# Kernel optimization log

Measured on AMD Instinct MI355X. Metric: run time of the kernel, lower is better.

## Reference

```python
import jax, jax.numpy as jnp
import numpy as np

B, CIN, CF, FH, FW = 16, 512, 64, 11, 20
N = 2784          # anchors
NOFF = 72         # S offsets
D = CF * FH       # 704

def setup_inputs() -> dict:
    key = jax.random.key(0)
    ks = jax.random.split(key, 12)
    x = jax.random.normal(ks[0], (B, CIN, FH, FW), jnp.float32)
    conv_w = jax.random.normal(ks[1], (CF, CIN), jnp.float32) * 0.02
    conv_b = jax.random.normal(ks[2], (CF,), jnp.float32) * 0.01
    attn_w = jax.random.normal(ks[3], (N - 1, D), jnp.float32) * 0.02
    attn_b = jnp.zeros((N - 1,), jnp.float32)
    cls_w = jax.random.normal(ks[4], (2, 2 * D), jnp.float32) * 0.02
    cls_b = jnp.zeros((2,), jnp.float32)
    reg_w = jax.random.normal(ks[5], (NOFF + 1, 2 * D), jnp.float32) * 0.02
    reg_b = jnp.zeros((NOFF + 1,), jnp.float32)
    anchors = jax.random.normal(ks[6], (N, 5 + NOFF), jnp.float32)
    # emulate compute_anchor_cut_indices: per-anchor per-fmap-row x index, some invalid
    unclamped = jax.random.randint(ks[7], (N, FH), -3, FW + 3, jnp.int32)
    invalid_mask = (unclamped < 0) | (unclamped > FW)
    cut_xs = jnp.clip(unclamped, 0, FW - 1).astype(jnp.int32)
    return {"x": x, "conv_w": conv_w, "conv_b": conv_b, "attn_w": attn_w,
            "attn_b": attn_b, "cls_w": cls_w, "cls_b": cls_b, "reg_w": reg_w,
            "reg_b": reg_b, "anchors": anchors, "cut_xs": cut_xs,
            "invalid_mask": invalid_mask}

def reference(x, conv_w, conv_b, attn_w, attn_b, cls_w, cls_b, reg_w, reg_b,
              anchors, cut_xs, invalid_mask):
    # 1x1 conv: [B, CF, FH, FW]
    feat = jnp.einsum('bchw,oc->bohw', x, conv_w) + conv_b[None, :, None, None]
    # cut_anchor_features: gather per-anchor column of features, mask invalid
    ys = jnp.arange(FH)[None, :]                      # [1, FH] broadcasts with cut_xs [N, FH]
    rois = feat[:, :, ys, cut_xs]                     # [B, CF, N, FH]
    rois = jnp.where(invalid_mask[None, None], 0.0, rois)
    anchor_feat = jnp.transpose(rois, (0, 2, 1, 3)).reshape(B, N, D)  # (C-major, then H)
    # attention scores over other anchors
    scores = anchor_feat.reshape(B * N, D) @ attn_w.T + attn_b
    att = jax.nn.softmax(scores, axis=1).reshape(B, N, N - 1)
    # build NxN matrix: zero diagonal, off-diagonal filled row-wise with att
    r = jnp.arange(N)[:, None]
    c = jnp.arange(N)[None, :]
    k = jnp.clip(c - (c > r).astype(jnp.int32), 0, N - 2)  # [N, N]
    M = att[:, r, k] * (c != r)                       # [B, N, N]
    att_feat = jnp.einsum('bij,bjd->bid', M, anchor_feat)
    comb = jnp.concatenate([att_feat, anchor_feat], axis=-1)  # [B, N, 2D]
    cls = comb @ cls_w.T + cls_b                      # [B, N, 2]
    reg = comb @ reg_w.T + reg_b                      # [B, N, 73]
    mid = jnp.broadcast_to(anchors[None, :, 2:4], (B, N, 2))
    props = jnp.concatenate([cls, mid, anchors[None, :, 4:] + reg], axis=-1)  # [B, N, 77]
    return props, M
```

## Files before the change

### kernel.cpp

```cpp
#include <hip/hip_runtime.h>

#define B_    16
#define CIN_  512
#define CF_   64
#define FH_   11
#define FW_   20
#define N_    2784
#define NM1_  2783
#define PK_   2816
#define D_    704
#define D2_   1408
#define ROWS_ 44544
#define PW_   77

#define NX_     1802240
#define NCW_    32768
#define NCB_    64
#define NATTW_  1959232
#define NATTB_  2783
#define NCLSW_  2816
#define NCLSB_  2
#define NREGW_  102784
#define NREGB_  73
#define NANCH_  214368
#define NCUT_   30624

#define OFF_FLAGS   0u
#define OFF_FEAT    256u
#define OFF_CANON   (1u<<20)
#define C_X      0u
#define C_ATTW   3604480u
#define C_CW     7522944u
#define C_ANCH   7588480u
#define C_CLSW   8017216u
#define C_REGW   8022848u
#define C_CB     8228416u
#define C_ATTB   8228544u
#define C_CLSB   8234112u
#define C_REGB   8234128u
#define C_CUT    8234288u
#define C_MASK   8356784u

typedef __bf16 bf16x8 __attribute__((ext_vector_type(8)));
typedef float  f32x4  __attribute__((ext_vector_type(4)));

typedef __attribute__((address_space(1))) void g_void;
typedef __attribute__((address_space(3))) void l_void;
#define GLD16(gp, lp) __builtin_amdgcn_global_load_lds((g_void*)(gp), (l_void*)(lp), 16, 0, 0)

__device__ __forceinline__ float bf2f(unsigned short u) {
    union { unsigned int u; float f; } v; v.u = ((unsigned int)u) << 16; return v.f;
}
__device__ __forceinline__ unsigned short f2bf(float f) {
    union { float f; unsigned int u; } v; v.f = f;
    unsigned int x = v.u;
    return (unsigned short)((x + 0x7FFFu + ((x >> 16) & 1u)) >> 16);
}

__device__ __forceinline__ int swz8(int olid, int nwg) {
    int xcd = olid & 7, pos = olid >> 3;
    int q = nwg >> 3, r = nwg & 7;
    int off = (xcd < r) ? xcd * (q + 1) : r * (q + 1) + (xcd - r) * q;
    return off + pos;
}

__global__ __launch_bounds__(256) void k_detect(const unsigned int* __restrict__ attw,
                                                const unsigned int* __restrict__ cut,
                                                const unsigned int* __restrict__ msk,
                                                int* __restrict__ flags) {
    __shared__ int cnt[3];
    int t = threadIdx.x;
    if (t < 3) cnt[t] = 0;
    __syncthreads();
    int c0 = 0, c1 = 0, c2 = 0;
    for (int i = t; i < 2048; i += 256) {
        unsigned int e = (attw[i] >> 7) & 0xFFu;
        if (e >= 127u) c0++;
    }
    for (int i = t; i < 4096; i += 256) if (cut[i] >= 32u) c1++;
    for (int i = t; i < 4096; i += 256) if (msk[i] >= 2u)  c2++;
    atomicAdd(&cnt[0], c0); atomicAdd(&cnt[1], c1); atomicAdd(&cnt[2], c2);
    __syncthreads();
    if (t == 0) {
        flags[0] = cnt[0] > 64;
        flags[1] = cnt[1] > 64;
        flags[2] = cnt[2] > 64;
        flags[3] = 0;
    }
}

__device__ __forceinline__ void cvt_arr(const void* s, unsigned short* d, int n, int isf32,
                                        int tid, int stride) {
    if (isf32) {
        const float* p = (const float*)s;
        for (int i = tid; i < n; i += stride) d[i] = f2bf(p[i]);
    } else {
        const unsigned short* p = (const unsigned short*)s;
        for (int i = tid; i < n; i += stride) d[i] = p[i];
    }
}

__global__ __launch_bounds__(256) void k_canon_f(const void* sx, const void* scw, const void* scb,
                                                 const void* sattw, const void* sattb,
                                                 const void* sclsw, const void* sclsb,
                                                 const void* sregw, const void* sregb,
                                                 const void* sanch, char* canon,
                                                 const int* __restrict__ flags) {
    const int isf32 = flags[0];
    const int tid = blockIdx.x * 256 + threadIdx.x;
    const int stride = gridDim.x * 256;
    cvt_arr(sx,    (unsigned short*)(canon + C_X),    NX_,    isf32, tid, stride);
    cvt_arr(sattw, (unsigned short*)(canon + C_ATTW), NATTW_, isf32, tid, stride);
    cvt_arr(scw,   (unsigned short*)(canon + C_CW),   NCW_,   isf32, tid, stride);
    cvt_arr(sanch, (unsigned short*)(canon + C_ANCH), NANCH_, isf32, tid, stride);
    cvt_arr(sclsw, (unsigned short*)(canon + C_CLSW), NCLSW_, isf32, tid, stride);
    cvt_arr(sregw, (unsigned short*)(canon + C_REGW), NREGW_, isf32, tid, stride);
    cvt_arr(scb,   (unsigned short*)(canon + C_CB),   NCB_,   isf32, tid, stride);
    cvt_arr(sattb, (unsigned short*)(canon + C_ATTB), NATTB_, isf32, tid, stride);
    cvt_arr(sclsb, (unsigned short*)(canon + C_CLSB), NCLSB_, isf32, tid, stride);
    cvt_arr(sregb, (unsigned short*)(canon + C_REGB), NREGB_, isf32, tid, stride);
}

__global__ __launch_bounds__(256) void k_canon_i(const void* scut, const void* smsk,
                                                 char* canon, const int* __restrict__ flags) {
    const int cutb = flags[1], mskb = flags[2];
    int* ccut = (int*)(canon + C_CUT);
    int* cmsk = (int*)(canon + C_MASK);
    const int tid = blockIdx.x * 256 + threadIdx.x;
    const int stride = gridDim.x * 256;
    for (int i = tid; i < NCUT_; i += stride) {
        ccut[i] = cutb ? (int)((const unsigned char*)scut)[i] : ((const int*)scut)[i];
        int m = mskb ? (int)((const unsigned char*)smsk)[i] : ((const int*)smsk)[i];
        cmsk[i] = (m != 0);
    }
}

__global__ __launch_bounds__(256) void k_conv(const unsigned short* __restrict__ x,
                                              const unsigned short* __restrict__ cw,
                                              const unsigned short* __restrict__ cb,
                                              float* __restrict__ feat) {
    int idx = blockIdx.x * 256 + threadIdx.x;
    int w = idx % FW_;
    int h = (idx / FW_) % FH_;
    int o = (idx / (FW_ * FH_)) % CF_;
    int b = idx / (FW_ * FH_ * CF_);
    const unsigned short* xp = x + ((size_t)(b * CIN_) * FH_ + h) * FW_ + w;
    const unsigned short* wp = cw + (size_t)o * CIN_;
    float acc = bf2f(cb[o]);
#pragma unroll 8
    for (int c = 0; c < CIN_; ++c)
        acc += bf2f(xp[(size_t)c * (FH_ * FW_)]) * bf2f(wp[c]);
    feat[idx] = acc;
}

__global__ __launch_bounds__(256) void k_gather_af(const float* __restrict__ feat,
                                                   const int* __restrict__ cut,
                                                   const int* __restrict__ inv,
                                                   unsigned short* __restrict__ AF,
                                                   int batch_base) {
    int n = blockIdx.x, bl = blockIdx.y;
    int b = batch_base + bl;
    __shared__ int cu[FH_];
    __shared__ int iv[FH_];
    int t = threadIdx.x;
    if (t < FH_) { cu[t] = cut[n * FH_ + t]; iv[t] = inv[n * FH_ + t]; }
    __syncthreads();
    unsigned short* out = AF + ((size_t)(bl * N_ + n)) * D_;
    for (int d = t; d < D_; d += 256) {
        int c = d / FH_, h = d - c * FH_;
        float v = iv[h] ? 0.f : feat[((b * CF_ + c) * FH_ + h) * FW_ + cu[h]];
        out[d] = f2bf(v);
    }
}

__global__ __launch_bounds__(256) void k_gather_aft(const float* __restrict__ feat,
                                                    const int* __restrict__ cut,
                                                    const int* __restrict__ inv,
                                                    unsigned short* __restrict__ AFT,
                                                    int batch_base) {
    int d = blockIdx.x, bl = blockIdx.y;
    int b = batch_base + bl;
    int c = d / FH_, h = d - c * FH_;
    const float* fp = feat + ((b * CF_ + c) * FH_ + h) * FW_;
    unsigned short* out = AFT + ((size_t)(bl * D_ + d)) * PK_;
    for (int n = threadIdx.x; n < PK_; n += 256) {
        float v = 0.f;
        if (n < N_) {
            int w = cut[n * FH_ + h];
            v = inv[n * FH_ + h] ? 0.f : fp[w];
        }
        out[n] = f2bf(v);
    }
}

__global__ __launch_bounds__(512, 1) void k_scores(const unsigned short* __restrict__ AF,
                                                   const unsigned short* __restrict__ attw,
                                                   const unsigned short* __restrict__ attb,
                                                   unsigned short* __restrict__ Mbf,
                                                   int nloc) {
    __shared__ __bf16 As[2][256 * 64];
    __shared__ __bf16 Bs[2][256 * 64];
    const int t = threadIdx.x;
    const int nwg = gridDim.x * gridDim.y;
    const int olid = blockIdx.x + gridDim.x * blockIdx.y;
    const int nid = swz8(olid, nwg);
    const int jt = nid % 11, it = nid / 11;
    const int i0 = it * 256, j0 = jt * 256;
    const int lane = t & 63, wv = t >> 6;
    const int wrow = wv >> 2, wcol = wv & 3;
    const int l15 = lane & 15, hi = lane >> 4;

    f32x4 zero = {0.f, 0.f, 0.f, 0.f};
    f32x4 acc[8][4];
#pragma unroll
    for (int m = 0; m < 8; ++m)
#pragma unroll
        for (int n = 0; n < 4; ++n) acc[m][n] = zero;

    const unsigned short* aP[4];
    const unsigned short* bP[4];
#pragma unroll
    for (int k = 0; k < 4; ++k) {
        int s = t + 512 * k;
        int row = s >> 3;
        int lc = (s & 7) ^ (row & 7);
        int ir = i0 + row; if (ir > nloc - 1) ir = nloc - 1;
        aP[k] = AF + (size_t)ir * D_ + lc * 8;
        int jr = j0 + row; if (jr > NM1_ - 1) jr = NM1_ - 1;
        bP[k] = attw + (size_t)jr * D_ + lc * 8;
    }

    const int NT = D_ / 64;
#pragma unroll
    for (int k = 0; k < 4; ++k) {
        GLD16(aP[k], As[0] + (t + 512 * k) * 8);
        GLD16(bP[k], Bs[0] + (t + 512 * k) * 8);
    }
    asm volatile("s_waitcnt vmcnt(0)" ::: "memory");
    __builtin_amdgcn_sched_barrier(0);
    __builtin_amdgcn_s_barrier();

    int cur = 0;
    for (int kt = 0; kt < NT; ++kt) {
        if (kt + 1 < NT) {
            const int nk = (kt + 1) * 64;
#pragma unroll
            for (int k = 0; k < 4; ++k) {
                GLD16(aP[k] + nk, As[cur ^ 1] + (t + 512 * k) * 8);
                GLD16(bP[k] + nk, Bs[cur ^ 1] + (t + 512 * k) * 8);
            }
        }
#pragma unroll
        for (int h = 0; h < 2; ++h) {
            bf16x8 a[8], bb[4];
#pragma unroll
            for (int m = 0; m < 8; ++m) {
                int R = wrow * 128 + m * 16 + l15;
                int pc = (hi + 4 * h) ^ (R & 7);
                a[m] = *(const bf16x8*)(As[cur] + R * 64 + pc * 8);
            }
#pragma unroll
            for (int n = 0; n < 4; ++n) {
                int R = wcol * 64 + n * 16 + l15;
                int pc = (hi + 4 * h) ^ (R & 7);
                bb[n] = *(const bf16x8*)(Bs[cur] + R * 64 + pc * 8);
            }
#pragma unroll
            for (int m = 0; m < 8; ++m)
#pragma unroll
                for (int n = 0; n < 4; ++n)
                    acc[m][n] = __builtin_amdgcn_mfma_f32_16x16x32_bf16(a[m], bb[n], acc[m][n], 0, 0, 0);
        }
        asm volatile("s_waitcnt vmcnt(0)" ::: "memory");
        __builtin_amdgcn_sched_barrier(0);
        __builtin_amdgcn_s_barrier();
        cur ^= 1;
    }

#pragma unroll
    for (int m = 0; m < 8; ++m) {
        int ib = i0 + wrow * 128 + m * 16 + hi * 4;
#pragma unroll
        for (int n = 0; n < 4; ++n) {
            int j = j0 + wcol * 64 + n * 16 + l15;
            if (j < NM1_) {
                float bias = bf2f(attb[j]);
#pragma unroll
                for (int q = 0; q < 4; ++q) {
                    int ii = ib + q;
                    if (ii < nloc) {
                        int r = ii % N_;
                        int c = j + (j >= r);
                        Mbf[(size_t)ii * PK_ + c] = f2bf(acc[m][n][q] + bias);
                    }
                }
            }
        }
    }
}

__global__ __launch_bounds__(256) void k_softmax(unsigned short* __restrict__ Mbf,
                                                 float* __restrict__ Mout,
                                                 int row_base) {
    const int il = blockIdx.x;
    const int r = il % N_;
    unsigned short* srow = Mbf + (size_t)il * PK_;
    float* orow = Mout + (size_t)(row_base + il) * N_;
    const int t = threadIdx.x;
    float f[16];
#pragma unroll
    for (int q = 0; q < 2; ++q) {
        int c8 = t + 256 * q;
        if (c8 < N_ / 8) {
            uint4 u = *(const uint4*)(srow + c8 * 8);
            const unsigned short* pu = (const unsigned short*)&u;
#pragma unroll
            for (int e = 0; e < 8; ++e) {
                int c = c8 * 8 + e;
                float v = bf2f(pu[e]);
                f[q * 8 + e] = (c == r) ? -1e30f : v;
            }
        } else {
#pragma unroll
            for (int e = 0; e < 8; ++e) f[q * 8 + e] = -1e30f;
        }
    }
    float m = -1e30f;
#pragma unroll
    for (int q = 0; q < 16; ++q) m = fmaxf(m, f[q]);
#pragma unroll
    for (int off = 32; off >= 1; off >>= 1) m = fmaxf(m, __shfl_xor(m, off, 64));
    __shared__ float red[4];
    if ((t & 63) == 0) red[t >> 6] = m;
    __syncthreads();
    m = fmaxf(fmaxf(red[0], red[1]), fmaxf(red[2], red[3]));

    float s = 0.f;
#pragma unroll
    for (int q = 0; q < 16; ++q) { float e = __expf(f[q] - m); f[q] = e; s += e; }
#pragma unroll
    for (int off = 32; off >= 1; off >>= 1) s += __shfl_xor(s, off, 64);
    __shared__ float red2[4];
    if ((t & 63) == 0) red2[t >> 6] = s;
    __syncthreads();
    s = red2[0] + red2[1] + red2[2] + red2[3];
    float inv = 1.0f / s;
#pragma unroll
    for (int q = 0; q < 2; ++q) {
        int c8 = t + 256 * q;
        if (c8 < N_ / 8) {
            float o[8];
            union { unsigned short u[8]; uint4 v; } pb;
#pragma unroll
            for (int e = 0; e < 8; ++e) {
                o[e] = f[q * 8 + e] * inv;
                pb.u[e] = f2bf(o[e]);
            }
            float4 o0 = {o[0], o[1], o[2], o[3]};
            float4 o1 = {o[4], o[5], o[6], o[7]};
            *(float4*)(orow + c8 * 8) = o0;
            *(float4*)(orow + c8 * 8 + 4) = o1;
            *(uint4*)(srow + c8 * 8) = pb.v;
        }
    }
    if (t < 4) {
        uint4 z = {0u, 0u, 0u, 0u};
        *(uint4*)(srow + N_ + t * 8) = z;
    }
}

__global__ __launch_bounds__(512, 1) void k_attgemm(const unsigned short* __restrict__ Mbf,
                                                    const unsigned short* __restrict__ AFT,
                                                    unsigned short* __restrict__ ATF) {
    __shared__ __bf16 As[2][256 * 64];
    __shared__ __bf16 Bs[2][256 * 64];
    const int t = threadIdx.x;
    const int nwg = gridDim.x * gridDim.y * gridDim.z;
    const int olid = blockIdx.x + gridDim.x * (blockIdx.y + gridDim.y * blockIdx.z);
    const int nid = swz8(olid, nwg);
    const int jt = nid % 3, it = (nid / 3) % 11, bl = nid / 33;
    const int i0 = it * 256, j0 = jt * 256;
    const int lane = t & 63, wv = t >> 6;
    const int wrow = wv >> 2, wcol = wv & 3;
    const int l15 = lane & 15, hi = lane >> 4;

    f32x4 zero = {0.f, 0.f, 0.f, 0.f};
    f32x4 acc[8][4];
#pragma unroll
    for (int m = 0; m < 8; ++m)
#pragma unroll
        for (int n = 0; n < 4; ++n) acc[m][n] = zero;

    const unsigned short* aP[4];
    const unsigned short* bP[4];
#pragma unroll
    for (int k = 0; k < 4; ++k) {
        int s = t + 512 * k;
        int row = s >> 3;
        int lc = (s & 7) ^ (row & 7);
        int ir = i0 + row; if (ir > N_ - 1) ir = N_ - 1;
        aP[k] = Mbf + ((size_t)bl * N_ + ir) * PK_ + lc * 8;
        int jr = j0 + row; if (jr > D_ - 1) jr = D_ - 1;
        bP[k] = AFT + ((size_t)bl * D_ + jr) * PK_ + lc * 8;
    }

    const int NT = PK_ / 64;
#pragma unroll
    for (int k = 0; k < 4; ++k) {
        GLD16(aP[k], As[0] + (t + 512 * k) * 8);
        GLD16(bP[k], Bs[0] + (t + 512 * k) * 8);
    }
    asm volatile("s_waitcnt vmcnt(0)" ::: "memory");
    __builtin_amdgcn_sched_barrier(0);
    __builtin_amdgcn_s_barrier();

    int cur = 0;
    for (int kt = 0; kt < NT; ++kt) {
        if (kt + 1 < NT) {
            const int nk = (kt + 1) * 64;
#pragma unroll
            for (int k = 0; k < 4; ++k) {
                GLD16(aP[k] + nk, As[cur ^ 1] + (t + 512 * k) * 8);
                GLD16(bP[k] + nk, Bs[cur ^ 1] + (t + 512 * k) * 8);
            }
        }
#pragma unroll
        for (int h = 0; h < 2; ++h) {
            bf16x8 a[8], bb[4];
#pragma unroll
            for (int m = 0; m < 8; ++m) {
                int R = wrow * 128 + m * 16 + l15;
                int pc = (hi + 4 * h) ^ (R & 7);
                a[m] = *(const bf16x8*)(As[cur] + R * 64 + pc * 8);
            }
#pragma unroll
            for (int n = 0; n < 4; ++n) {
                int R = wcol * 64 + n * 16 + l15;
                int pc = (hi + 4 * h) ^ (R & 7);
                bb[n] = *(const bf16x8*)(Bs[cur] + R * 64 + pc * 8);
            }
#pragma unroll
            for (int m = 0; m < 8; ++m)
#pragma unroll
                for (int n = 0; n < 4; ++n)
                    acc[m][n] = __builtin_amdgcn_mfma_f32_16x16x32_bf16(a[m], bb[n], acc[m][n], 0, 0, 0);
        }
        asm volatile("s_waitcnt vmcnt(0)" ::: "memory");
        __builtin_amdgcn_sched_barrier(0);
        __builtin_amdgcn_s_barrier();
        cur ^= 1;
    }

#pragma unroll
    for (int m = 0; m < 8; ++m) {
        int rb = i0 + wrow * 128 + m * 16 + hi * 4;
#pragma unroll
        for (int n = 0; n < 4; ++n) {
            int d = j0 + wcol * 64 + n * 16 + l15;
            if (d < D_) {
#pragma unroll
                for (int q = 0; q < 4; ++q) {
                    int rr = rb + q;
                    if (rr < N_)
                        ATF[((size_t)(bl * N_ + rr)) * D_ + d] = f2bf(acc[m][n][q]);
                }
            }
        }
    }
}

__global__ __launch_bounds__(256) void k_head(const unsigned short* __restrict__ ATF,
                                              const unsigned short* __restrict__ AF,
                                              const unsigned short* __restrict__ clsw,
                                              const unsigned short* __restrict__ clsb,
                                              const unsigned short* __restrict__ regw,
                                              const unsigned short* __restrict__ regb,
                                              const unsigned short* __restrict__ anch,
                                              float* __restrict__ props,
                                              int row_base, int nloc) {
    __shared__ __bf16 As[128 * 32];
    __shared__ __bf16 Ws[80 * 32];
    const int t = threadIdx.x;
    const int i0 = blockIdx.x * 128;
    const int lane = t & 63, wv = t >> 6;
    const int l15 = lane & 15, hi8 = (lane >> 4) * 8;

    f32x4 zero = {0.f, 0.f, 0.f, 0.f};
    f32x4 acc[2][5];
#pragma unroll
    for (int m = 0; m < 2; ++m)
#pragma unroll
        for (int n = 0; n < 5; ++n) acc[m][n] = zero;

    const int s0 = t, s1 = t + 256;
    const int ar0 = s0 >> 2, ac0 = (s0 & 3) * 8;
    const int ar1 = s1 >> 2, ac1 = (s1 & 3) * 8;
    int ir0 = i0 + ar0; if (ir0 > nloc - 1) ir0 = nloc - 1;
    int ir1 = i0 + ar1; if (ir1 > nloc - 1) ir1 = nloc - 1;
    const unsigned short* w0base = (ar0 < 2) ? (clsw + (size_t)ar0 * D2_)
                                             : (regw + (size_t)(ar0 - 2) * D2_);
    int r1 = 64 + (t >> 2);
    int rc = r1 < 75 ? r1 : 74;
    const unsigned short* w1base = regw + (size_t)(rc - 2) * D2_;
    const int w1c = (t & 3) * 8;

    for (int p = 0; p < 2; ++p) {
        const unsigned short* Asrc = (p == 0) ? ATF : AF;
        const int wcol = p * D_;
        for (int k0 = 0; k0 < D_; k0 += 32) {
            GLD16(Asrc + (size_t)ir0 * D_ + ac0 + k0, As + s0 * 8);
            GLD16(Asrc + (size_t)ir1 * D_ + ac1 + k0, As + s1 * 8);
            GLD16(w0base + wcol + k0 + ac0, Ws + s0 * 8);
            if (t < 64) GLD16(w1base + wcol + k0 + w1c, Ws + (size_t)(256 + t) * 8);
            __syncthreads();
            bf16x8 a[2], bb[5];
#pragma unroll
            for (int m = 0; m < 2; ++m)
                a[m] = *(const bf16x8*)(As + (wv * 32 + m * 16 + l15) * 32 + hi8);
#pragma unroll
            for (int n = 0; n < 5; ++n)
                bb[n] = *(const bf16x8*)(Ws + (n * 16 + l15) * 32 + hi8);
#pragma unroll
            for (int m = 0; m < 2; ++m)
#pragma unroll
                for (int n = 0; n < 5; ++n)
                    acc[m][n] = __builtin_amdgcn_mfma_f32_16x16x32_bf16(a[m], bb[n], acc[m][n], 0, 0, 0);
            __syncthreads();
        }
    }

#pragma unroll
    for (int m = 0; m < 2; ++m) {
        int ib = i0 + wv * 32 + m * 16 + (lane >> 4) * 4;
#pragma unroll
        for (int n = 0; n < 5; ++n) {
            int j = n * 16 + l15;
            if (j < 75) {
#pragma unroll
                for (int q = 0; q < 4; ++q) {
                    int i = ib + q;
                    if (i < nloc) {
                        size_t g = (size_t)(row_base + i);
                        int nn = i % N_;
                        float v = acc[m][n][q];
                        if (j < 2) {
                            props[g * PW_ + j] = v + bf2f(clsb[j]);
                            props[g * PW_ + 2 + j] = bf2f(anch[(size_t)nn * PW_ + 2 + j]);
                        } else {
                            int tt = j - 2;
                            props[g * PW_ + 4 + tt] = v + bf2f(regb[tt]) + bf2f(anch[(size_t)nn * PW_ + 4 + tt]);
                        }
                    }
                }
            }
        }
    }
}

extern "C" void kernel_launch(void* const* d_in, const int* in_sizes, int n_in,
                              void* d_out, int out_size, void* d_ws, size_t ws_size,
                              hipStream_t stream) {
    (void)in_sizes; (void)n_in; (void)out_size;

    float* props = (float*)d_out;
    float* Mbuf  = props + (size_t)ROWS_ * PW_;

    char* ws = (char*)d_ws;
    int* flags = (int*)(ws + OFF_FLAGS);
    float* feat = (float*)(ws + OFF_FEAT);
    char* canon = ws + OFF_CANON;
    unsigned short* cx    = (unsigned short*)(canon + C_X);
    unsigned short* cattw = (unsigned short*)(canon + C_ATTW);
    unsigned short* ccw   = (unsigned short*)(canon + C_CW);
    unsigned short* canch = (unsigned short*)(canon + C_ANCH);
    unsigned short* cclsw = (unsigned short*)(canon + C_CLSW);
    unsigned short* cregw = (unsigned short*)(canon + C_REGW);
    unsigned short* ccb   = (unsigned short*)(canon + C_CB);
    unsigned short* cattb = (unsigned short*)(canon + C_ATTB);
    unsigned short* cclsb = (unsigned short*)(canon + C_CLSB);
    unsigned short* cregb = (unsigned short*)(canon + C_REGB);
    int* ccut = (int*)(canon + C_CUT);
    int* cmsk = (int*)(canon + C_MASK);

    const size_t base = (size_t)(12u << 20);
    const size_t per  = ((size_t)N_ * D_ * 2) * 2 + (size_t)D_ * PK_ * 2 + (size_t)N_ * PK_ * 2;
    int CN = 1;
    for (int c = 16; c >= 1; c >>= 1)
        if (ws_size >= base + (size_t)c * per) { CN = c; break; }
    unsigned short* AF  = (unsigned short*)(ws + base);
    unsigned short* AFT = AF  + (size_t)CN * N_ * D_;
    unsigned short* ATF = AFT + (size_t)CN * D_ * PK_;
    unsigned short* Mbf = ATF + (size_t)CN * N_ * D_;

    k_detect<<<dim3(1), dim3(256), 0, stream>>>((const unsigned int*)d_in[3],
                                                (const unsigned int*)d_in[10],
                                                (const unsigned int*)d_in[11], flags);
    k_canon_f<<<dim3(1024), dim3(256), 0, stream>>>(d_in[0], d_in[1], d_in[2], d_in[3], d_in[4],
                                                    d_in[5], d_in[6], d_in[7], d_in[8], d_in[9],
                                                    canon, flags);
    k_canon_i<<<dim3(120), dim3(256), 0, stream>>>(d_in[10], d_in[11], canon, flags);
    k_conv<<<dim3(880), dim3(256), 0, stream>>>(cx, ccw, ccb, feat);

    const int nchunk = 16 / CN;
    for (int c = 0; c < nchunk; ++c) {
        const int bb = c * CN;
        const int rb = bb * N_;
        const int nl = CN * N_;
        const int it128 = (nl + 127) / 128;
        const int it256 = (nl + 255) / 256;
        k_gather_af<<<dim3(N_, CN), dim3(256), 0, stream>>>(feat, ccut, cmsk, AF, bb);
        k_gather_aft<<<dim3(D_, CN), dim3(256), 0, stream>>>(feat, ccut, cmsk, AFT, bb);
        k_scores<<<dim3(11, it256), dim3(512), 0, stream>>>(AF, cattw, cattb, Mbf, nl);
        k_softmax<<<dim3(nl), dim3(256), 0, stream>>>(Mbf, Mbuf, rb);
        k_attgemm<<<dim3(3, 11, CN), dim3(512), 0, stream>>>(Mbf, AFT, ATF);
        k_head<<<dim3(it128), dim3(256), 0, stream>>>(ATF, AF, cclsw, cclsb, cregw, cregb,
                                                      canch, props, rb, nl);
    }
}
```

Measured before the change: 1.097 ms.

## Split GEMM K-tiles into half stages with finer-grained pipelined loads and MFMA priority

Both big GEMM kernels (scores and attention-weighted features) now stage each 64-wide K tile as two 32-wide halves. Loads for upcoming halves are interleaved between MFMA groups, and vmcnt(8) waits replace full drains, so global-to-LDS copies overlap compute at finer granularity. The LDS swizzle changes to a 4-chunk XOR pattern, and s_setprio raises wave priority around MFMA bursts. This adds more barriers per tile and relies on correct waitcnt accounting, which risks stalls or races if the counts are off.

```diff
diff --git a/kernel.cpp b/kernel.cpp
--- a/kernel.cpp
+++ b/kernel.cpp
@@ -47,6 +47,8 @@
 typedef __attribute__((address_space(1))) void g_void;
 typedef __attribute__((address_space(3))) void l_void;
 #define GLD16(gp, lp) __builtin_amdgcn_global_load_lds((g_void*)(gp), (l_void*)(lp), 16, 0, 0)
+
+#define G2(r) (((r) + ((r) >> 2)) & 3)
 
 __device__ __forceinline__ float bf2f(unsigned short u) {
     union { unsigned int u; float f; } v; v.u = ((unsigned int)u) << 16; return v.f;
@@ -193,13 +195,81 @@
     }
 }
 
+
+#define GEMM_PROLOGUE()                                                               \
+    STAGE_A(0, 0, 0); STAGE_B(0, 0, 0); STAGE_A(0, 1, 0); STAGE_B(0, 1, 0);           \
+    STAGE_A(1, 0, 1); STAGE_B(1, 0, 1);
+
+#define RD_A(kh)                                                                      \
+    _Pragma("unroll")                                                                 \
+    for (int m = 0; m < 8; ++m) {                                                     \
+        int R = wrow * 128 + m * 16 + l15;                                            \
+        a[m] = *(const bf16x8*)(As + cur * 16384 + (kh) * 8192 + R * 32 +             \
+                                ((hi ^ G2(R)) * 8));                                  \
+    }
+
+#define RD_B(kh, n0)                                                                  \
+    {                                                                                 \
+        int R0 = wcol * 64 + (n0) * 16 + l15;                                         \
+        int R1 = wcol * 64 + ((n0) + 1) * 16 + l15;                                   \
+        b0 = *(const bf16x8*)(Bs + cur * 16384 + (kh) * 8192 + R0 * 32 +              \
+                              ((hi ^ G2(R0)) * 8));                                   \
+        b1 = *(const bf16x8*)(Bs + cur * 16384 + (kh) * 8192 + R1 * 32 +              \
+                              ((hi ^ G2(R1)) * 8));                                   \
+    }
+
+#define MFMA16(n0)                                                                    \
+    asm volatile("s_waitcnt lgkmcnt(0)" ::: "memory");                                \
+    __builtin_amdgcn_sched_barrier(0);                                                \
+    __builtin_amdgcn_s_setprio(1);                                                    \
+    _Pragma("unroll")                                                                 \
+    for (int m = 0; m < 8; ++m) {                                                     \
+        acc[m][(n0)] = __builtin_amdgcn_mfma_f32_16x16x32_bf16(a[m], b0, acc[m][(n0)], 0, 0, 0); \
+        acc[m][(n0) + 1] = __builtin_amdgcn_mfma_f32_16x16x32_bf16(a[m], b1, acc[m][(n0) + 1], 0, 0, 0); \
+    }                                                                                 \
+    __builtin_amdgcn_s_setprio(0);
+
+#define BOUNDARY(tail)                                                                \
+    if (tail) asm volatile("s_waitcnt vmcnt(0)" ::: "memory");                        \
+    else      asm volatile("s_waitcnt vmcnt(8)" ::: "memory");                        \
+    __builtin_amdgcn_sched_barrier(0);                                                \
+    __builtin_amdgcn_s_barrier();
+
+#define GEMM_LOOP(NT)                                                                 \
+    for (int tt = 0; tt < (NT); ++tt) {                                               \
+        const int cur = tt & 1, nxt = cur ^ 1;                                        \
+        const bool tail = (tt >= (NT) - 2);                                           \
+        BOUNDARY(tail);                                                               \
+                                                                  \
+        RD_A(0); RD_B(0, 0);                                                          \
+        if (tt + 1 < (NT)) STAGE_A(nxt, 1, tt + 1);                                   \
+        MFMA16(0);                                                                    \
+        __builtin_amdgcn_s_barrier();                                                 \
+                                                                  \
+        RD_B(0, 2);                                                                   \
+        if (tt + 1 < (NT)) STAGE_B(nxt, 1, tt + 1);                                   \
+        MFMA16(2);                                                                    \
+        __builtin_amdgcn_s_barrier();                                                 \
+        BOUNDARY(tail);                                                               \
+                                                                  \
+        RD_A(1); RD_B(1, 0);                                                          \
+        if (tt + 2 < (NT)) STAGE_A(cur, 0, tt + 2);                                   \
+        MFMA16(0);                                                                    \
+        __builtin_amdgcn_s_barrier();                                                 \
+                                                                  \
+        RD_B(1, 2);                                                                   \
+        if (tt + 2 < (NT)) STAGE_B(cur, 0, tt + 2);                                   \
+        MFMA16(2);                                                                    \
+                                      \
+    }
+
 __global__ __launch_bounds__(512, 1) void k_scores(const unsigned short* __restrict__ AF,
                                                    const unsigned short* __restrict__ attw,
                                                    const unsigned short* __restrict__ attb,
                                                    unsigned short* __restrict__ Mbf,
                                                    int nloc) {
-    __shared__ __bf16 As[2][256 * 64];
-    __shared__ __bf16 Bs[2][256 * 64];
+    __shared__ __bf16 As[2 * 16384];
+    __shared__ __bf16 Bs[2 * 16384];
     const int t = threadIdx.x;
     const int nwg = gridDim.x * gridDim.y;
     const int olid = blockIdx.x + gridDim.x * blockIdx.y;
@@ -217,65 +287,32 @@
 #pragma unroll
         for (int n = 0; n < 4; ++n) acc[m][n] = zero;
 
-    const unsigned short* aP[4];
-    const unsigned short* bP[4];
-#pragma unroll
-    for (int k = 0; k < 4; ++k) {
-        int s = t + 512 * k;
-        int row = s >> 3;
-        int lc = (s & 7) ^ (row & 7);
-        int ir = i0 + row; if (ir > nloc - 1) ir = nloc - 1;
-        aP[k] = AF + (size_t)ir * D_ + lc * 8;
-        int jr = j0 + row; if (jr > NM1_ - 1) jr = NM1_ - 1;
-        bP[k] = attw + (size_t)jr * D_ + lc * 8;
-    }
-
-    const int NT = D_ / 64;
-#pragma unroll
-    for (int k = 0; k < 4; ++k) {
-        GLD16(aP[k], As[0] + (t + 512 * k) * 8);
-        GLD16(bP[k], Bs[0] + (t + 512 * k) * 8);
-    }
-    asm volatile("s_waitcnt vmcnt(0)" ::: "memory");
-    __builtin_amdgcn_sched_barrier(0);
-    __builtin_amdgcn_s_barrier();
-
-    int cur = 0;
-    for (int kt = 0; kt < NT; ++kt) {
-        if (kt + 1 < NT) {
-            const int nk = (kt + 1) * 64;
-#pragma unroll
-            for (int k = 0; k < 4; ++k) {
-                GLD16(aP[k] + nk, As[cur ^ 1] + (t + 512 * k) * 8);
-                GLD16(bP[k] + nk, Bs[cur ^ 1] + (t + 512 * k) * 8);
-            }
-        }
-#pragma unroll
-        for (int h = 0; h < 2; ++h) {
-            bf16x8 a[8], bb[4];
-#pragma unroll
-            for (int m = 0; m < 8; ++m) {
-                int R = wrow * 128 + m * 16 + l15;
-                int pc = (hi + 4 * h) ^ (R & 7);
-                a[m] = *(const bf16x8*)(As[cur] + R * 64 + pc * 8);
-            }
-#pragma unroll
-            for (int n = 0; n < 4; ++n) {
-                int R = wcol * 64 + n * 16 + l15;
-                int pc = (hi + 4 * h) ^ (R & 7);
-                bb[n] = *(const bf16x8*)(Bs[cur] + R * 64 + pc * 8);
-            }
-#pragma unroll
-            for (int m = 0; m < 8; ++m)
-#pragma unroll
-                for (int n = 0; n < 4; ++n)
-                    acc[m][n] = __builtin_amdgcn_mfma_f32_16x16x32_bf16(a[m], bb[n], acc[m][n], 0, 0, 0);
-        }
-        asm volatile("s_waitcnt vmcnt(0)" ::: "memory");
-        __builtin_amdgcn_sched_barrier(0);
-        __builtin_amdgcn_s_barrier();
-        cur ^= 1;
-    }
+    const unsigned short *aB0, *aB1, *bB0, *bB1;
+    {
+        int s0 = t, s1 = t + 512;
+        int r0 = s0 >> 2, r1 = s1 >> 2;
+        int lc0 = (s0 & 3) ^ G2(r0), lc1 = (s1 & 3) ^ G2(r1);
+        int ia0 = i0 + r0; if (ia0 > nloc - 1) ia0 = nloc - 1;
+        int ia1 = i0 + r1; if (ia1 > nloc - 1) ia1 = nloc - 1;
+        int jb0 = j0 + r0; if (jb0 > NM1_ - 1) jb0 = NM1_ - 1;
+        int jb1 = j0 + r1; if (jb1 > NM1_ - 1) jb1 = NM1_ - 1;
+        aB0 = AF + (size_t)ia0 * D_ + lc0 * 8;
+        aB1 = AF + (size_t)ia1 * D_ + lc1 * 8;
+        bB0 = attw + (size_t)jb0 * D_ + lc0 * 8;
+        bB1 = attw + (size_t)jb1 * D_ + lc1 * 8;
+    }
+#define STAGE_A(buf, kh, kt) { \
+    GLD16(aB0 + (kt) * 64 + (kh) * 32, As + (buf) * 16384 + (kh) * 8192 + t * 8); \
+    GLD16(aB1 + (kt) * 64 + (kh) * 32, As + (buf) * 16384 + (kh) * 8192 + (t + 512) * 8); }
+#define STAGE_B(buf, kh, kt) { \
+    GLD16(bB0 + (kt) * 64 + (kh) * 32, Bs + (buf) * 16384 + (kh) * 8192 + t * 8); \
+    GLD16(bB1 + (kt) * 64 + (kh) * 32, Bs + (buf) * 16384 + (kh) * 8192 + (t + 512) * 8); }
+
+    bf16x8 a[8], b0, b1;
+    GEMM_PROLOGUE();
+    GEMM_LOOP(11);
+#undef STAGE_A
+#undef STAGE_B
 
 #pragma unroll
     for (int m = 0; m < 8; ++m) {
@@ -372,8 +409,8 @@
 __global__ __launch_bounds__(512, 1) void k_attgemm(const unsigned short* __restrict__ Mbf,
                                                     const unsigned short* __restrict__ AFT,
                                                     unsigned short* __restrict__ ATF) {
-    __shared__ __bf16 As[2][256 * 64];
-    __shared__ __bf16 Bs[2][256 * 64];
+    __shared__ __bf16 As[2 * 16384];
+    __shared__ __bf16 Bs[2 * 16384];
     const int t = threadIdx.x;
     const int nwg = gridDim.x * gridDim.y * gridDim.z;
     const int olid = blockIdx.x + gridDim.x * (blockIdx.y + gridDim.y * blockIdx.z);
@@ -391,65 +428,32 @@
 #pragma unroll
         for (int n = 0; n < 4; ++n) acc[m][n] = zero;
 
-    const unsigned short* aP[4];
-    const unsigned short* bP[4];
-#pragma unroll
-    for (int k = 0; k < 4; ++k) {
-        int s = t + 512 * k;
-        int row = s >> 3;
-        int lc = (s & 7) ^ (row & 7);
-        int ir = i0 + row; if (ir > N_ - 1) ir = N_ - 1;
-        aP[k] = Mbf + ((size_t)bl * N_ + ir) * PK_ + lc * 8;
-        int jr = j0 + row; if (jr > D_ - 1) jr = D_ - 1;
-        bP[k] = AFT + ((size_t)bl * D_ + jr) * PK_ + lc * 8;
-    }
-
-    const int NT = PK_ / 64;
-#pragma unroll
-    for (int k = 0; k < 4; ++k) {
-        GLD16(aP[k], As[0] + (t + 512 * k) * 8);
-        GLD16(bP[k], Bs[0] + (t + 512 * k) * 8);
-    }
-    asm volatile("s_waitcnt vmcnt(0)" ::: "memory");
-    __builtin_amdgcn_sched_barrier(0);
-    __builtin_amdgcn_s_barrier();
-
-    int cur = 0;
-    for (int kt = 0; kt < NT; ++kt) {
-        if (kt + 1 < NT) {
-            const int nk = (kt + 1) * 64;
-#pragma unroll
-            for (int k = 0; k < 4; ++k) {
-                GLD16(aP[k] + nk, As[cur ^ 1] + (t + 512 * k) * 8);
-                GLD16(bP[k] + nk, Bs[cur ^ 1] + (t + 512 * k) * 8);
-            }
-        }
-#pragma unroll
-        for (int h = 0; h < 2; ++h) {
-            bf16x8 a[8], bb[4];
-#pragma unroll
-            for (int m = 0; m < 8; ++m) {
-                int R = wrow * 128 + m * 16 + l15;
-                int pc = (hi + 4 * h) ^ (R & 7);
-                a[m] = *(const bf16x8*)(As[cur] + R * 64 + pc * 8);
-            }
-#pragma unroll
-            for (int n = 0; n < 4; ++n) {
-                int R = wcol * 64 + n * 16 + l15;
-                int pc = (hi + 4 * h) ^ (R & 7);
-                bb[n] = *(const bf16x8*)(Bs[cur] + R * 64 + pc * 8);
-            }
-#pragma unroll
-            for (int m = 0; m < 8; ++m)
-#pragma unroll
-                for (int n = 0; n < 4; ++n)
-                    acc[m][n] = __builtin_amdgcn_mfma_f32_16x16x32_bf16(a[m], bb[n], acc[m][n], 0, 0, 0);
-        }
-        asm volatile("s_waitcnt vmcnt(0)" ::: "memory");
-        __builtin_amdgcn_sched_barrier(0);
-        __builtin_amdgcn_s_barrier();
-        cur ^= 1;
-    }
+    const unsigned short *aB0, *aB1, *bB0, *bB1;
+    {
+        int s0 = t, s1 = t + 512;
+        int r0 = s0 >> 2, r1 = s1 >> 2;
+        int lc0 = (s0 & 3) ^ G2(r0), lc1 = (s1 & 3) ^ G2(r1);
+        int ia0 = i0 + r0; if (ia0 > N_ - 1) ia0 = N_ - 1;
+        int ia1 = i0 + r1; if (ia1 > N_ - 1) ia1 = N_ - 1;
+        int jb0 = j0 + r0; if (jb0 > D_ - 1) jb0 = D_ - 1;
+        int jb1 = j0 + r1; if (jb1 > D_ - 1) jb1 = D_ - 1;
+        aB0 = Mbf + ((size_t)bl * N_ + ia0) * PK_ + lc0 * 8;
+        aB1 = Mbf + ((size_t)bl * N_ + ia1) * PK_ + lc1 * 8;
+        bB0 = AFT + ((size_t)bl * D_ + jb0) * PK_ + lc0 * 8;
+        bB1 = AFT + ((size_t)bl * D_ + jb1) * PK_ + lc1 * 8;
+    }
+#define STAGE_A(buf, kh, kt) { \
+    GLD16(aB0 + (kt) * 64 + (kh) * 32, As + (buf) * 16384 + (kh) * 8192 + t * 8); \
+    GLD16(aB1 + (kt) * 64 + (kh) * 32, As + (buf) * 16384 + (kh) * 8192 + (t + 512) * 8); }
+#define STAGE_B(buf, kh, kt) { \
+    GLD16(bB0 + (kt) * 64 + (kh) * 32, Bs + (buf) * 16384 + (kh) * 8192 + t * 8); \
+    GLD16(bB1 + (kt) * 64 + (kh) * 32, Bs + (buf) * 16384 + (kh) * 8192 + (t + 512) * 8); }
+
+    bf16x8 a[8], b0, b1;
+    GEMM_PROLOGUE();
+    GEMM_LOOP(44);
+#undef STAGE_A
+#undef STAGE_B
 
 #pragma unroll
     for (int m = 0; m < 8; ++m) {
@@ -478,7 +482,7 @@
                                               const unsigned short* __restrict__ anch,
                                               float* __restrict__ props,
                                               int row_base, int nloc) {
-    __shared__ __bf16 As[128 * 32];
+    __shared__ __bf16 As2[128 * 32];
     __shared__ __bf16 Ws[80 * 32];
     const int t = threadIdx.x;
     const int i0 = blockIdx.x * 128;
@@ -508,15 +512,15 @@
         const unsigned short* Asrc = (p == 0) ? ATF : AF;
         const int wcol = p * D_;
         for (int k0 = 0; k0 < D_; k0 += 32) {
-            GLD16(Asrc + (size_t)ir0 * D_ + ac0 + k0, As + s0 * 8);
-            GLD16(Asrc + (size_t)ir1 * D_ + ac1 + k0, As + s1 * 8);
+            GLD16(Asrc + (size_t)ir0 * D_ + ac0 + k0, As2 + s0 * 8);
+            GLD16(Asrc + (size_t)ir1 * D_ + ac1 + k0, As2 + s1 * 8);
             GLD16(w0base + wcol + k0 + ac0, Ws + s0 * 8);
             if (t < 64) GLD16(w1base + wcol + k0 + w1c, Ws + (size_t)(256 + t) * 8);
             __syncthreads();
             bf16x8 a[2], bb[5];
 #pragma unroll
             for (int m = 0; m < 2; ++m)
-                a[m] = *(const bf16x8*)(As + (wv * 32 + m * 16 + l15) * 32 + hi8);
+                a[m] = *(const bf16x8*)(As2 + (wv * 32 + m * 16 + l15) * 32 + hi8);
 #pragma unroll
             for (int n = 0; n < 5; ++n)
                 bb[n] = *(const bf16x8*)(Ws + (n * 16 + l15) * 32 + hi8);
```

Measured after the change: 994.9 us. -9.3%, faster.
